# Kernel optimization log

Hardware: AMD Instinct MI355X
Metric: run time of the kernel (lower is better)

Reference implementation:

```python
import jax, jax.numpy as jnp
import numpy as np

M, IN, OUT = 8192, 4096, 4096
BITWIDTH = 7


def psto_shift_int32(x, shift):
    """Pseudo-stochastic right-shift of int32 x by `shift` bits -> int8.
    Faithful to PstoShiftInt32: floor-divide, derive a pseudo random number
    from the low half of the remainder, compare against the high half."""
    pow_s = jnp.left_shift(jnp.int32(1), shift)
    rt = jnp.floor_divide(x, pow_s)
    prob = jnp.abs(x - rt * pow_s)
    half_pow = jnp.left_shift(jnp.int32(1), shift // 2)
    qp = jnp.floor_divide(prob, half_pow)
    prn = prob - qp * half_pow
    prn = jnp.where(shift % 2 == 1, prn * 2, prn)
    dec = jnp.where(qp <= prn, jnp.int32(0), jnp.int32(1)) * jnp.sign(x)
    return jnp.clip(rt + dec, -127, 127).astype(jnp.int8)


def range_bitwidth(x):
    # RangeEstimate: ceil(log2(max|x|)), 0 if all-zero (torch also goes via float)
    m = jnp.max(jnp.abs(x)).astype(jnp.float32)
    return jnp.where(m == 0, jnp.int32(0), jnp.ceil(jnp.log2(m)).astype(jnp.int32))


def act_calc(acc, exp_in):
    """Shift int32 accumulator back to int8 and track the block exponent."""
    bw = range_bitwidth(acc)
    shift = bw - BITWIDTH
    # shift>1 -> shift by `shift`; shift==1 -> shift by 2; else -> plain int8 cast
    eff = jnp.where(shift > 1, shift, jnp.where(shift == 1, jnp.int32(2), jnp.int32(0)))
    rounded = psto_shift_int32(acc, jnp.maximum(eff, 0))
    out = jnp.where(eff > 0, rounded, acc.astype(jnp.int8))  # int8 cast wraps, as in torch
    exp_out = (exp_in + eff).astype(jnp.int8)
    return out, exp_out


def setup_inputs() -> dict:
    key = jax.random.key(0)
    k1, k2 = jax.random.split(key)
    # int8-valued tensors kept in int32 containers for the matmul accumulate
    act_in = jax.random.randint(k1, (M, IN), -127, 128, dtype=jnp.int32)
    weight = jax.random.randint(k2, (OUT, IN), -127, 128, dtype=jnp.int32)
    return {"act_in": act_in, "exp_in": -6, "weight": weight, "weight_exp": -9}


def reference(act_in, exp_in, weight, weight_exp):
    # the roundoff4 padding in the original is a no-op)
    acc = jnp.matmul(act_in, weight.T)  # [M, OUT] int32
    act_out, exp_out = act_calc(acc, jnp.int32(exp_in) + jnp.int32(weight_exp))
    return act_out, exp_out
```

## Files before the change

### kernel.cpp

```cpp
#include <hip/hip_runtime.h>
#include <stdint.h>
#include <math.h>

#define M_DIM 8192
#define N_DIM 4096
#define K_DIM 4096
#define BITWIDTH 7

#define BM 256
#define BN 128
#define BK 128

using i32x4  = __attribute__((ext_vector_type(4)))  int;
using i32x16 = __attribute__((ext_vector_type(16))) int;

__global__ __launch_bounds__(256) void pack_both_kernel(
        const int* __restrict__ act, const int* __restrict__ wt,
        uint32_t* __restrict__ act8, uint32_t* __restrict__ w8,
        int* __restrict__ maxabs) {
    if (blockIdx.x == 0 && threadIdx.x == 0) *maxabs = 0;
    const int ACT_N8 = (M_DIM * K_DIM) / 8;
    int i = blockIdx.x * blockDim.x + threadIdx.x;
    const int* src;
    uint32_t* dst;
    if (i < ACT_N8) { src = act; dst = act8; }
    else            { src = wt;  dst = w8;  i -= ACT_N8; }
    int4 a = ((const int4*)src)[2 * i];
    int4 b = ((const int4*)src)[2 * i + 1];
    uint32_t p0 = (uint32_t)(a.x & 0xFF) | ((uint32_t)(a.y & 0xFF) << 8)
                | ((uint32_t)(a.z & 0xFF) << 16) | ((uint32_t)(a.w & 0xFF) << 24);
    uint32_t p1 = (uint32_t)(b.x & 0xFF) | ((uint32_t)(b.y & 0xFF) << 8)
                | ((uint32_t)(b.z & 0xFF) << 16) | ((uint32_t)(b.w & 0xFF) << 24);
    ((uint2*)dst)[i] = make_uint2(p0, p1);
}

__device__ __forceinline__ void gload_lds16(const int8_t* g, int8_t* lds) {
    __builtin_amdgcn_global_load_lds(
        (__attribute__((address_space(1))) void*)g,
        (__attribute__((address_space(3))) void*)lds,
        16, 0, 0);
}

__global__ __launch_bounds__(256, 2) void gemm_i8(
        const int8_t* __restrict__ A8, const int8_t* __restrict__ B8,
        int* __restrict__ C, int* __restrict__ maxabs) {
    __shared__ __align__(16) int8_t As[BM * BK];
    __shared__ __align__(16) int8_t Bs[BN * BK];
    __shared__ int wmaxs[4];

    const int tid  = threadIdx.x;
    const int wave = tid >> 6;
    const int lane = tid & 63;

    const int row0 = blockIdx.y * BM;
    const int col0 = blockIdx.x * BN;

    const int wm = (wave >> 1) * 128;
    const int wn = (wave & 1) * 64;

    i32x16 acc[4][2];
#pragma unroll
    for (int i = 0; i < 4; ++i)
#pragma unroll
        for (int j = 0; j < 2; ++j)
            acc[i][j] = (i32x16)(0);

    const int raA    = wave * 64;
    const int raB    = wave * 32;
    const int rowoff = lane >> 3;
    const int chk    = ((lane & 7) ^ rowoff) << 4;

    const int8_t* ag = A8 + (size_t)(row0 + raA + rowoff) * K_DIM + chk;
    const int8_t* bg = B8 + (size_t)(col0 + raB + rowoff) * K_DIM + chk;

    const int fr  = lane & 31;
    const int hl  = lane >> 5;
    const int swz = fr & 7;
    int aoff[4][4], boff[2][4];
#pragma unroll
    for (int kk = 0; kk < 4; ++kk) {
        int co = (((kk * 2 + hl) ^ swz) << 4);
#pragma unroll
        for (int i = 0; i < 4; ++i)
            aoff[i][kk] = (wm + i * 32 + fr) * BK + co;
#pragma unroll
        for (int j = 0; j < 2; ++j)
            boff[j][kk] = (wn + j * 32 + fr) * BK + co;
    }

    for (int k0 = 0; k0 < K_DIM; k0 += BK) {
        __syncthreads();
#pragma unroll
        for (int g = 0; g < 8; ++g)
            gload_lds16(ag + k0 + (size_t)(8 * g) * K_DIM, As + (raA + 8 * g) * BK);
#pragma unroll
        for (int g = 0; g < 4; ++g)
            gload_lds16(bg + k0 + (size_t)(8 * g) * K_DIM, Bs + (raB + 8 * g) * BK);
        __syncthreads();

#pragma unroll
        for (int kk = 0; kk < 4; ++kk) {
            i32x4 af[4], bf[2];
#pragma unroll
            for (int i = 0; i < 4; ++i)
                af[i] = *(const i32x4*)(As + aoff[i][kk]);
#pragma unroll
            for (int j = 0; j < 2; ++j)
                bf[j] = *(const i32x4*)(Bs + boff[j][kk]);
#pragma unroll
            for (int i = 0; i < 4; ++i)
#pragma unroll
                for (int j = 0; j < 2; ++j)
                    acc[i][j] = __builtin_amdgcn_mfma_i32_32x32x32_i8(
                        af[i], bf[j], acc[i][j], 0, 0, 0);
        }
    }

    int mymax = 0;
    const int ccol = lane & 31;
    const int rbase = hl << 2;
#pragma unroll
    for (int i = 0; i < 4; ++i) {
#pragma unroll
        for (int j = 0; j < 2; ++j) {
            int* p = C + (size_t)(row0 + wm + i * 32) * N_DIM
                       + (col0 + wn + j * 32 + ccol);
#pragma unroll
            for (int r = 0; r < 16; ++r) {
                int row = (r & 3) + 8 * (r >> 2) + rbase;
                int v = acc[i][j][r];
                p[(size_t)row * N_DIM] = v;
                int a = v < 0 ? -v : v;
                mymax = a > mymax ? a : mymax;
            }
        }
    }

#pragma unroll
    for (int off = 32; off > 0; off >>= 1) {
        int o = __shfl_down(mymax, off, 64);
        mymax = o > mymax ? o : mymax;
    }
    if (lane == 0) wmaxs[wave] = mymax;
    __syncthreads();
    if (tid == 0) {
        int bmx = wmaxs[0];
        for (int w = 1; w < 4; ++w) bmx = wmaxs[w] > bmx ? wmaxs[w] : bmx;
        atomicMax(maxabs, bmx);
    }
}

__device__ __forceinline__ int psto(int x, int eff) {
    if (eff > 0) {
        int rt   = x >> eff;
        int prob = x & ((1 << eff) - 1);
        int h    = eff >> 1;
        int qp   = prob >> h;
        int prn  = (prob & ((1 << h) - 1)) << (eff & 1);
        int sgn  = (x > 0) - (x < 0);
        int r    = rt + ((qp <= prn) ? 0 : sgn);
        r = r < -127 ? -127 : r;
        r = r > 127 ? 127 : r;
        return r;
    }
    return (int)(int8_t)x;
}

__global__ __launch_bounds__(256) void finalize_kernel(int* __restrict__ C,
        const int* __restrict__ maxabs,
        const int* __restrict__ exp_in,
        const int* __restrict__ wexp) {
    const int m = *maxabs;
    int bw = 0;
    if (m != 0) bw = (int)ceilf(log2f((float)m));
    const int shift = bw - BITWIDTH;
    const int eff = (shift > 1) ? shift : ((shift == 1) ? 2 : 0);

    const size_t idx = ((size_t)blockIdx.x * blockDim.x + threadIdx.x) * 8;
    int4 v0 = *(const int4*)(C + idx);
    int4 v1 = *(const int4*)(C + idx + 4);
    int4 o0, o1;
    o0.x = psto(v0.x, eff); o0.y = psto(v0.y, eff);
    o0.z = psto(v0.z, eff); o0.w = psto(v0.w, eff);
    o1.x = psto(v1.x, eff); o1.y = psto(v1.y, eff);
    o1.z = psto(v1.z, eff); o1.w = psto(v1.w, eff);
    *(int4*)(C + idx) = o0;
    *(int4*)(C + idx + 4) = o1;

    if (idx == 0) {
        C[(size_t)M_DIM * N_DIM] = (int)(int8_t)(exp_in[0] + wexp[0] + eff);
    }
}

extern "C" void kernel_launch(void* const* d_in, const int* in_sizes, int n_in,
                              void* d_out, int out_size, void* d_ws, size_t ws_size,
                              hipStream_t stream) {
    const int* act    = (const int*)d_in[0];
    const int* exp_in = (const int*)d_in[1];
    const int* wt     = (const int*)d_in[2];
    const int* wexp   = (const int*)d_in[3];

    int8_t* act8   = (int8_t*)d_ws;
    int8_t* w8     = act8 + (size_t)M_DIM * K_DIM;
    int*    maxabs = (int*)(w8 + (size_t)N_DIM * K_DIM);

    pack_both_kernel<<<24576, 256, 0, stream>>>(
        act, wt, (uint32_t*)act8, (uint32_t*)w8, maxabs);

    int* C = (int*)d_out;
    dim3 grid(N_DIM / BN, M_DIM / BM);
    gemm_i8<<<grid, 256, 0, stream>>>(act8, w8, C, maxabs);

    finalize_kernel<<<((size_t)M_DIM * N_DIM / 8) / 256, 256, 0, stream>>>(
        C, maxabs, exp_in, wexp);
}
```

Measured before the change: 450.8 us.

## Rework int8 GEMM into 256x256 tiles with 4-stage LDS pipeline and XCD remap

The int8 GEMM moves from 256x128 tiles with 256 threads and a single-buffered BK=128 loop to 256x256 tiles with 512 threads. It adds a 4-deep ring of KT=64 LDS stages that is prefetched with global_load_lds, plus manual vmcnt/lgkmcnt waits, barriers and s_setprio around the MFMA bursts. Block indices are remapped so blocks on the same XCD share tiles in L2. The aim is to hide global-load latency behind compute and raise operand reuse, at the cost of a larger dynamic LDS footprint and a hand-tuned wait schedule that is fragile.

```diff
diff --git a/kernel.cpp b/kernel.cpp
--- a/kernel.cpp
+++ b/kernel.cpp
@@ -8,8 +8,10 @@
 #define BITWIDTH 7
 
 #define BM 256
-#define BN 128
-#define BK 128
+#define BN 256
+#define KT 64
+#define NT (K_DIM / KT)
+#define TILEB (BM * KT)
 
 using i32x4  = __attribute__((ext_vector_type(4)))  int;
 using i32x16 = __attribute__((ext_vector_type(16))) int;
@@ -41,22 +43,29 @@
         16, 0, 0);
 }
 
-__global__ __launch_bounds__(256, 2) void gemm_i8(
+__global__ __launch_bounds__(512, 2) void gemm_i8(
         const int8_t* __restrict__ A8, const int8_t* __restrict__ B8,
         int* __restrict__ C, int* __restrict__ maxabs) {
-    __shared__ __align__(16) int8_t As[BM * BK];
-    __shared__ __align__(16) int8_t Bs[BN * BK];
-    __shared__ int wmaxs[4];
+    extern __shared__ int8_t smem[];
+    int8_t* As = smem;
+    int8_t* Bs = smem + 4 * TILEB;
 
     const int tid  = threadIdx.x;
     const int wave = tid >> 6;
     const int lane = tid & 63;
-
-    const int row0 = blockIdx.y * BM;
-    const int col0 = blockIdx.x * BN;
-
-    const int wm = (wave >> 1) * 128;
-    const int wn = (wave & 1) * 64;
+    const int fr   = lane & 31;
+    const int hl   = lane >> 5;
+
+    const int orig = blockIdx.x;
+    const int xcd  = orig & 7;
+    const int idx  = orig >> 3;
+    const int bx   = xcd * 2 + (idx >> 5);
+    const int by   = idx & 31;
+
+    const int row0 = by * BM;
+    const int col0 = bx * BN;
+    const int wm   = (wave >> 2) * 128;
+    const int wn   = (wave & 3) * 64;
 
     i32x16 acc[4][2];
 #pragma unroll
@@ -65,59 +74,90 @@
         for (int j = 0; j < 2; ++j)
             acc[i][j] = (i32x16)(0);
 
-    const int raA    = wave * 64;
-    const int raB    = wave * 32;
-    const int rowoff = lane >> 3;
-    const int chk    = ((lane & 7) ^ rowoff) << 4;
-
-    const int8_t* ag = A8 + (size_t)(row0 + raA + rowoff) * K_DIM + chk;
-    const int8_t* bg = B8 + (size_t)(col0 + raB + rowoff) * K_DIM + chk;
-
-    const int fr  = lane & 31;
-    const int hl  = lane >> 5;
-    const int swz = fr & 7;
-    int aoff[4][4], boff[2][4];
-#pragma unroll
-    for (int kk = 0; kk < 4; ++kk) {
-        int co = (((kk * 2 + hl) ^ swz) << 4);
+    const int srow = wave * 16 + (lane >> 2);
+    const int schk = ((lane & 3) ^ ((lane >> 3) & 3)) << 4;
+    const int8_t* aS = A8 + (size_t)(row0 + srow) * K_DIM + schk;
+    const int8_t* bS = B8 + (size_t)(col0 + srow) * K_DIM + schk;
+    const int ldso = wave * 1024;
+
+    int aoff[2][4], boff[2][2];
+#pragma unroll
+    for (int kk = 0; kk < 2; ++kk) {
+        const int slot = ((2 * kk + hl) ^ ((fr >> 1) & 3)) << 4;
 #pragma unroll
         for (int i = 0; i < 4; ++i)
-            aoff[i][kk] = (wm + i * 32 + fr) * BK + co;
+            aoff[kk][i] = (wm + i * 32 + fr) * KT + slot;
 #pragma unroll
         for (int j = 0; j < 2; ++j)
-            boff[j][kk] = (wn + j * 32 + fr) * BK + co;
-    }
-
-    for (int k0 = 0; k0 < K_DIM; k0 += BK) {
-        __syncthreads();
-#pragma unroll
-        for (int g = 0; g < 8; ++g)
-            gload_lds16(ag + k0 + (size_t)(8 * g) * K_DIM, As + (raA + 8 * g) * BK);
-#pragma unroll
-        for (int g = 0; g < 4; ++g)
-            gload_lds16(bg + k0 + (size_t)(8 * g) * K_DIM, Bs + (raB + 8 * g) * BK);
-        __syncthreads();
-
-#pragma unroll
-        for (int kk = 0; kk < 4; ++kk) {
-            i32x4 af[4], bf[2];
-#pragma unroll
-            for (int i = 0; i < 4; ++i)
-                af[i] = *(const i32x4*)(As + aoff[i][kk]);
+            boff[kk][j] = (wn + j * 32 + fr) * KT + slot;
+    }
+
+#pragma unroll
+    for (int pt = 0; pt < 3; ++pt) {
+        const int sb = pt * TILEB;
+        const size_t ko = (size_t)pt * KT;
+        gload_lds16(aS + ko,                          As + sb + ldso);
+        gload_lds16(aS + ko + (size_t)128 * K_DIM,    As + sb + 8192 + ldso);
+        gload_lds16(bS + ko,                          Bs + sb + ldso);
+        gload_lds16(bS + ko + (size_t)128 * K_DIM,    Bs + sb + 8192 + ldso);
+    }
+    asm volatile("s_waitcnt vmcnt(8)" ::: "memory");
+    __builtin_amdgcn_s_barrier();
+
+    for (int t = 0; t < NT; ++t) {
+        const int rb = (t & 3) * TILEB;
+        const int sb = ((t + 3) & 3) * TILEB;
+        const size_t ko = (size_t)(t + 3) * KT;
+        const bool st = (t < NT - 3);
+
+        i32x4 af[4], bf[2];
+
+#pragma unroll
+        for (int i = 0; i < 4; ++i) af[i] = *(const i32x4*)(As + rb + aoff[0][i]);
+#pragma unroll
+        for (int j = 0; j < 2; ++j) bf[j] = *(const i32x4*)(Bs + rb + boff[0][j]);
+        if (st) {
+            gload_lds16(aS + ko,                       As + sb + ldso);
+            gload_lds16(aS + ko + (size_t)128 * K_DIM, As + sb + 8192 + ldso);
+        }
+        __builtin_amdgcn_s_barrier();
+        asm volatile("s_waitcnt lgkmcnt(0)" ::: "memory");
+        __builtin_amdgcn_s_setprio(1);
+#pragma unroll
+        for (int i = 0; i < 4; ++i)
 #pragma unroll
             for (int j = 0; j < 2; ++j)
-                bf[j] = *(const i32x4*)(Bs + boff[j][kk]);
-#pragma unroll
-            for (int i = 0; i < 4; ++i)
-#pragma unroll
-                for (int j = 0; j < 2; ++j)
-                    acc[i][j] = __builtin_amdgcn_mfma_i32_32x32x32_i8(
-                        af[i], bf[j], acc[i][j], 0, 0, 0);
-        }
+                acc[i][j] = __builtin_amdgcn_mfma_i32_32x32x32_i8(
+                    af[i], bf[j], acc[i][j], 0, 0, 0);
+        __builtin_amdgcn_s_setprio(0);
+        __builtin_amdgcn_s_barrier();
+
+#pragma unroll
+        for (int i = 0; i < 4; ++i) af[i] = *(const i32x4*)(As + rb + aoff[1][i]);
+#pragma unroll
+        for (int j = 0; j < 2; ++j) bf[j] = *(const i32x4*)(Bs + rb + boff[1][j]);
+        if (st) {
+            gload_lds16(bS + ko,                       Bs + sb + ldso);
+            gload_lds16(bS + ko + (size_t)128 * K_DIM, Bs + sb + 8192 + ldso);
+        }
+        if (t < NT - 3)       asm volatile("s_waitcnt vmcnt(8)" ::: "memory");
+        else if (t == NT - 3) asm volatile("s_waitcnt vmcnt(4)" ::: "memory");
+        else if (t == NT - 2) asm volatile("s_waitcnt vmcnt(0)" ::: "memory");
+        __builtin_amdgcn_s_barrier();
+        asm volatile("s_waitcnt lgkmcnt(0)" ::: "memory");
+        __builtin_amdgcn_s_setprio(1);
+#pragma unroll
+        for (int i = 0; i < 4; ++i)
+#pragma unroll
+            for (int j = 0; j < 2; ++j)
+                acc[i][j] = __builtin_amdgcn_mfma_i32_32x32x32_i8(
+                    af[i], bf[j], acc[i][j], 0, 0, 0);
+        __builtin_amdgcn_s_setprio(0);
+        __builtin_amdgcn_s_barrier();
     }
 
     int mymax = 0;
-    const int ccol = lane & 31;
+    const int ccol  = fr;
     const int rbase = hl << 2;
 #pragma unroll
     for (int i = 0; i < 4; ++i) {
@@ -141,11 +181,14 @@
         int o = __shfl_down(mymax, off, 64);
         mymax = o > mymax ? o : mymax;
     }
-    if (lane == 0) wmaxs[wave] = mymax;
+    if (lane == 0) ((volatile int*)smem)[wave] = mymax;
     __syncthreads();
     if (tid == 0) {
-        int bmx = wmaxs[0];
-        for (int w = 1; w < 4; ++w) bmx = wmaxs[w] > bmx ? wmaxs[w] : bmx;
+        int bmx = ((volatile int*)smem)[0];
+        for (int w = 1; w < 8; ++w) {
+            int x = ((volatile int*)smem)[w];
+            bmx = x > bmx ? x : bmx;
+        }
         atomicMax(maxabs, bmx);
     }
 }
@@ -204,12 +247,20 @@
     int8_t* w8     = act8 + (size_t)M_DIM * K_DIM;
     int*    maxabs = (int*)(w8 + (size_t)N_DIM * K_DIM);
 
+    static int cfg_done = 0;
+    if (!cfg_done) {
+        hipFuncSetAttribute(reinterpret_cast<const void*>(gemm_i8),
+                            hipFuncAttributeMaxDynamicSharedMemorySize,
+                            8 * TILEB);
+        cfg_done = 1;
+    }
+
     pack_both_kernel<<<24576, 256, 0, stream>>>(
         act, wt, (uint32_t*)act8, (uint32_t*)w8, maxabs);
 
     int* C = (int*)d_out;
-    dim3 grid(N_DIM / BN, M_DIM / BM);
-    gemm_i8<<<grid, 256, 0, stream>>>(act8, w8, C, maxabs);
+    gemm_i8<<<(M_DIM / BM) * (N_DIM / BN), 512, 8 * TILEB, stream>>>(
+        act8, w8, C, maxabs);
 
     finalize_kernel<<<((size_t)M_DIM * N_DIM / 8) / 256, 256, 0, stream>>>(
         C, maxabs, exp_in, wexp);
```

Measured after the change: 455.7 us. About the same (+1.1%).

## Load A fragments directly from global and double-buffer B in LDS

Applied to the files above, without the earlier changes.

The A tile is no longer staged through shared memory; each wave reads its A fragments straight from global memory into registers. B is now double-buffered in LDS, so the next B tile is prefetched while the current one is consumed, leaving one barrier per k-step instead of two. This cuts LDS footprint and synchronisation but turns A reads into uncoalesced 16-byte global loads. Those loads sit on the MFMA critical path with no software prefetch, and A data is shared between waves only through cache.

```diff
diff --git a/kernel.cpp b/kernel.cpp
--- a/kernel.cpp
+++ b/kernel.cpp
@@ -44,13 +44,14 @@
 __global__ __launch_bounds__(256, 2) void gemm_i8(
         const int8_t* __restrict__ A8, const int8_t* __restrict__ B8,
         int* __restrict__ C, int* __restrict__ maxabs) {
-    __shared__ __align__(16) int8_t As[BM * BK];
-    __shared__ __align__(16) int8_t Bs[BN * BK];
+    __shared__ __align__(16) int8_t Bs[2][BN * BK];
     __shared__ int wmaxs[4];
 
     const int tid  = threadIdx.x;
     const int wave = tid >> 6;
     const int lane = tid & 63;
+    const int fr   = lane & 31;
+    const int hl   = lane >> 5;
 
     const int row0 = blockIdx.y * BM;
     const int col0 = blockIdx.x * BN;
@@ -65,48 +66,49 @@
         for (int j = 0; j < 2; ++j)
             acc[i][j] = (i32x16)(0);
 
-    const int raA    = wave * 64;
-    const int raB    = wave * 32;
-    const int rowoff = lane >> 3;
-    const int chk    = ((lane & 7) ^ rowoff) << 4;
-
-    const int8_t* ag = A8 + (size_t)(row0 + raA + rowoff) * K_DIM + chk;
-    const int8_t* bg = B8 + (size_t)(col0 + raB + rowoff) * K_DIM + chk;
-
-    const int fr  = lane & 31;
-    const int hl  = lane >> 5;
+    const int srowoff = lane >> 3;
+    const int schk    = ((lane & 7) ^ srowoff) << 4;
+    const int8_t* bg  = B8 + (size_t)(col0 + wave * 8 + srowoff) * K_DIM + schk;
+    const int ldsoB   = wave * 1024;
+
+    const int8_t* agf = A8 + (size_t)(row0 + wm + fr) * K_DIM + hl * 16;
+
     const int swz = fr & 7;
-    int aoff[4][4], boff[2][4];
+    int boff[4][2];
 #pragma unroll
     for (int kk = 0; kk < 4; ++kk) {
-        int co = (((kk * 2 + hl) ^ swz) << 4);
-#pragma unroll
-        for (int i = 0; i < 4; ++i)
-            aoff[i][kk] = (wm + i * 32 + fr) * BK + co;
+        const int co = (((kk * 2 + hl) ^ swz) << 4);
 #pragma unroll
         for (int j = 0; j < 2; ++j)
-            boff[j][kk] = (wn + j * 32 + fr) * BK + co;
-    }
-
-    for (int k0 = 0; k0 < K_DIM; k0 += BK) {
-        __syncthreads();
-#pragma unroll
-        for (int g = 0; g < 8; ++g)
-            gload_lds16(ag + k0 + (size_t)(8 * g) * K_DIM, As + (raA + 8 * g) * BK);
-#pragma unroll
-        for (int g = 0; g < 4; ++g)
-            gload_lds16(bg + k0 + (size_t)(8 * g) * K_DIM, Bs + (raB + 8 * g) * BK);
-        __syncthreads();
+            boff[kk][j] = (wn + j * 32 + fr) * BK + co;
+    }
+
+#pragma unroll
+    for (int g = 0; g < 4; ++g)
+        gload_lds16(bg + (size_t)(32 * g) * K_DIM, Bs[0] + g * 4096 + ldsoB);
+    __syncthreads();
+
+    for (int t = 0; t < K_DIM / BK; ++t) {
+        const int k0  = t * BK;
+        const int buf = t & 1;
+
+        if (t < K_DIM / BK - 1) {
+#pragma unroll
+            for (int g = 0; g < 4; ++g)
+                gload_lds16(bg + k0 + BK + (size_t)(32 * g) * K_DIM,
+                            Bs[buf ^ 1] + g * 4096 + ldsoB);
+        }
 
 #pragma unroll
         for (int kk = 0; kk < 4; ++kk) {
             i32x4 af[4], bf[2];
 #pragma unroll
             for (int i = 0; i < 4; ++i)
-                af[i] = *(const i32x4*)(As + aoff[i][kk]);
+                af[i] = *(const i32x4*)(agf + (size_t)(i * 32) * K_DIM
+                                            + k0 + kk * 32);
 #pragma unroll
             for (int j = 0; j < 2; ++j)
-                bf[j] = *(const i32x4*)(Bs + boff[j][kk]);
+                bf[j] = *(const i32x4*)(Bs[buf] + boff[kk][j]);
 #pragma unroll
             for (int i = 0; i < 4; ++i)
 #pragma unroll
@@ -114,10 +116,11 @@
                     acc[i][j] = __builtin_amdgcn_mfma_i32_32x32x32_i8(
                         af[i], bf[j], acc[i][j], 0, 0, 0);
         }
+        __syncthreads();
     }
 
     int mymax = 0;
-    const int ccol = lane & 31;
+    const int ccol = fr;
     const int rbase = hl << 2;
 #pragma unroll
     for (int i = 0; i < 4; ++i) {
```

New measurement: 584.7 us. 29.7% more time.
